# Optimization experiments

Measured on AMD Instinct MI355X. Metric: run time of the kernel, lower is better.

## Reference

```python
import jax, jax.numpy as jnp
import numpy as np

N = 100000        # nodes
E = 1600000       # directed edges
F = 602           # Reddit num_features
D = 32            # EMBEDDING_SIZE
C = 41            # Reddit num_classes
BN_EPS = 1e-5


def setup_inputs() -> dict:
    key = jax.random.key(0)
    ks = jax.random.split(key, 24)
    def w(k, shape, fan_in):
        return jax.random.normal(k, shape, dtype=jnp.float32) * (1.0 / np.sqrt(fan_in))
    inp = {
        "x": jax.random.normal(ks[0], (N, F), dtype=jnp.float32),
        "edge_index": jax.random.randint(ks[1], (2, E), 0, N, dtype=jnp.int32),
        # lin1: F -> 2*D
        "lin1_w": w(ks[2], (F, 2 * D), F), "lin1_b": jnp.zeros((2 * D,), jnp.float32),
        # conv1 MLP: 2*D -> D -> D
        "nn1_w1": w(ks[3], (2 * D, D), 2 * D), "nn1_b1": jnp.zeros((D,), jnp.float32),
        "nn1_w2": w(ks[4], (D, D), D), "nn1_b2": jnp.zeros((D,), jnp.float32),
        "bn1_g": jnp.ones((D,), jnp.float32), "bn1_b": jnp.zeros((D,), jnp.float32),
        # conv2 MLP: D -> D -> D
        "nn2_w1": w(ks[5], (D, D), D), "nn2_b1": jnp.zeros((D,), jnp.float32),
        "nn2_w2": w(ks[6], (D, D), D), "nn2_b2": jnp.zeros((D,), jnp.float32),
        "bn2_g": jnp.ones((D,), jnp.float32), "bn2_b": jnp.zeros((D,), jnp.float32),
        # heads
        "fc1_w": w(ks[7], (D, D), D), "fc1_b": jnp.zeros((D,), jnp.float32),
        "fc2_w": w(ks[8], (D, C), D), "fc2_b": jnp.zeros((C,), jnp.float32),
    }
    return inp


def _gin_conv(x, src, dst, w1, b1, w2, b2, eps=0.0):
    # sum-aggregate neighbor features (adj_t @ x) then MLP
    agg = jax.ops.segment_sum(x[src], dst, num_segments=N)  # [N, d]
    h = (1.0 + eps) * x + agg
    h = jnp.maximum(h @ w1 + b1, 0.0) @ w2 + b2
    return h


def _batch_norm(x, gamma, beta):
    # training-mode BatchNorm1d: batch statistics, biased variance
    mu = jnp.mean(x, axis=0)
    var = jnp.mean(jnp.square(x - mu), axis=0)
    return (x - mu) * jax.lax.rsqrt(var + BN_EPS) * gamma + beta


def reference(x, edge_index, lin1_w, lin1_b,
              nn1_w1, nn1_b1, nn1_w2, nn1_b2, bn1_g, bn1_b,
              nn2_w1, nn2_b1, nn2_w2, nn2_b2, bn2_g, bn2_b,
              fc1_w, fc1_b, fc2_w, fc2_b):
    src, dst = edge_index[0], edge_index[1]
    h = x @ lin1_w + lin1_b                                  # [N, 64]
    h = _batch_norm(_gin_conv(h, src, dst, nn1_w1, nn1_b1, nn1_w2, nn1_b2), bn1_g, bn1_b)
    h = _batch_norm(_gin_conv(h, src, dst, nn2_w1, nn2_b1, nn2_w2, nn2_b2), bn2_g, bn2_b)
    h = jnp.maximum(h @ fc1_w + fc1_b, 0.0)
    return h @ fc2_w + fc2_b                                 # [N, C]
```

## Files before the change

kernel.cpp:

```cpp
#include <hip/hip_runtime.h>
#include <cstdint>

#define NN 100000
#define NE 1600000
#define FI 602
#define DD 32
#define CC 41
#define BN_EPS 1e-5f
#define KSTEPS 19

#define NPB 256
#define NB 391
#define BST 4608
#define EPT 13
#define SCB 481

typedef __attribute__((ext_vector_type(8))) short bf16x8;
typedef __attribute__((ext_vector_type(4))) float f32x4;

__device__ __forceinline__ void atomAdd(float* p, float v) {
#ifdef __HIP_PLATFORM_AMD__
  unsafeAtomicAdd(p, v);
#else
  atomicAdd(p, v);
#endif
}

__device__ __forceinline__ unsigned short f2b(float f) {
  unsigned u = __float_as_uint(f);
  unsigned r = (u + 0x7fffu + ((u >> 16) & 1u)) >> 16;
  return (unsigned short)r;
}
__device__ __forceinline__ float blo(unsigned u) { return __uint_as_float(u << 16); }
__device__ __forceinline__ float bhi(unsigned u) { return __uint_as_float(u & 0xffff0000u); }

__global__ __launch_bounds__(256) void k0_prep(
    const float* __restrict__ lin1_w, const float* __restrict__ lin1_b,
    const float* __restrict__ nn1_w1,
    unsigned short* __restrict__ Bh,
    float* __restrict__ cvec,
    float* __restrict__ stats1, float* __restrict__ stats2) {
  int o = blockIdx.x * 256 + threadIdx.x;
  if (o < KSTEPS * 32 * 32) {
    int k = o >> 5, j = o & 31;
    float s = 0.f;
    if (k < FI) {
      #pragma unroll 4
      for (int c = 0; c < 2 * DD; ++c) s = fmaf(lin1_w[k * (2 * DD) + c], nn1_w1[c * DD + j], s);
    }
    int st = k >> 5, kk = k & 31, g = kk >> 3, jj = kk & 7;
    int h = j >> 4, lane = g * 16 + (j & 15);
    int idx = ((st * 2 + h) * 64 + lane) * 8 + jj;
    Bh[idx] = f2b(s);
  }
  if (blockIdx.x == 0) {
    int t = threadIdx.x;
    if (t < DD) {
      float s = 0.f;
      for (int c = 0; c < 2 * DD; ++c) s = fmaf(lin1_b[c], nn1_w1[c * DD + t], s);
      cvec[t] = s;
    }
    if (t >= 128 && t < 192) stats1[t - 128] = 0.f;
    if (t >= 192) stats2[t - 192] = 0.f;
  }
}

__global__ __launch_bounds__(256) void kb_scatter(const int* __restrict__ ei,
                                                  int* __restrict__ bcursor,
                                                  int* __restrict__ tsrc,
                                                  unsigned char* __restrict__ tdst) {
  __shared__ int cnt[NB];
  __shared__ int wbase[NB];
  const int t = threadIdx.x;
  for (int i = t; i < NB; i += 256) cnt[i] = 0;
  __syncthreads();
  const int base = blockIdx.x * (256 * EPT);
  int s[EPT], d[EPT];
  #pragma unroll
  for (int i = 0; i < EPT; ++i) {
    int e = base + i * 256 + t;
    if (e < NE) {
      s[i] = ei[e];
      d[i] = ei[NE + e];
      atomicAdd(&cnt[d[i] >> 8], 1);
    } else {
      s[i] = -1; d[i] = -1;
    }
  }
  __syncthreads();
  for (int i = t; i < NB; i += 256) wbase[i] = atomicAdd(&bcursor[i], cnt[i]);
  __syncthreads();
  #pragma unroll
  for (int i = 0; i < EPT; ++i) {
    if (d[i] >= 0) {
      int bk = d[i] >> 8;
      int p = atomicAdd(&wbase[bk], 1);
      int gp = bk * BST + p;
      tsrc[gp] = s[i];
      tdst[gp] = (unsigned char)(d[i] & (NPB - 1));
    }
  }
}

__global__ __launch_bounds__(256) void kb_fine(const int* __restrict__ bcursor,
                                               const int* __restrict__ tsrc,
                                               const unsigned char* __restrict__ tdst,
                                               int* __restrict__ rs, int* __restrict__ re,
                                               int* __restrict__ srcidx) {
  __shared__ int deg[NPB];
  __shared__ int cur[NPB];
  __shared__ int woff[4];
  const int b = blockIdx.x, t = threadIdx.x;
  const int beg = b * BST;
  const int end = beg + bcursor[b];
  deg[t] = 0;
  __syncthreads();
  for (int i = beg + t; i < end; i += 256) atomicAdd(&deg[tdst[i]], 1);
  __syncthreads();
  int v = deg[t];
  int lane = t & 63, wave = t >> 6;
  int inc = v;
  #pragma unroll
  for (int off = 1; off < 64; off <<= 1) {
    int u = __shfl_up(inc, off);
    if (lane >= off) inc += u;
  }
  if (lane == 63) woff[wave] = inc;
  __syncthreads();
  int wadd = 0;
  for (int w = 0; w < wave; ++w) wadd += woff[w];
  int excl = wadd + inc - v;
  int gnode = b * NPB + t;
  if (gnode < NN) {
    rs[gnode] = beg + excl;
    re[gnode] = beg + excl + v;
  }
  cur[t] = beg + excl;
  __syncthreads();
  for (int i = beg + t; i < end; i += 256) {
    int p = atomicAdd(&cur[tdst[i]], 1);
    srcidx[p] = tsrc[i];
  }
}

__global__ __launch_bounds__(256) void k1_mfma(
    const float* __restrict__ x,
    const unsigned short* __restrict__ Bh,
    const float* __restrict__ cvec, unsigned short* __restrict__ zb) {
  __shared__ float part[2][64][9];
  const int tid = threadIdx.x;
  const int lane = tid & 63;
  const int w = tid >> 6;
  const int rg = w & 1;
  const int kh = w >> 1;
  const int row0 = blockIdx.x * 32 + rg * 16;
  const int g = lane >> 4;
  const int r = row0 + (lane & 15);
  const float* __restrict__ xr = x + (size_t)r * FI + g * 8;
  f32x4 acc0 = {0.f, 0.f, 0.f, 0.f};
  f32x4 acc1 = {0.f, 0.f, 0.f, 0.f};

  if (kh == 0) {
    float4 a0 = *(const float4*)&xr[0];
    float4 b0 = *(const float4*)&xr[4];
    float4 a1 = *(const float4*)&xr[32];
    float4 b1 = *(const float4*)&xr[36];
    bf16x8 f0c = *(const bf16x8*)&Bh[(size_t)lane * 8];
    bf16x8 f1c = *(const bf16x8*)&Bh[(size_t)lane * 8 + 512];
    #pragma unroll
    for (int s = 0; s < 10; ++s) {
      float4 ca = a0, cb = b0;
      a0 = a1; b0 = b1;
      if (s + 2 < 10) {
        a1 = *(const float4*)&xr[(s + 2) * 32];
        b1 = *(const float4*)&xr[(s + 2) * 32 + 4];
      }
      bf16x8 f0n, f1n;
      if (s + 1 < 10) {
        const size_t fb = ((size_t)((s + 1) * 2) * 64 + lane) * 8;
        f0n = *(const bf16x8*)&Bh[fb];
        f1n = *(const bf16x8*)&Bh[fb + 512];
      }
      bf16x8 ahi, alo;
      float cv0[8] = {ca.x, ca.y, ca.z, ca.w, cb.x, cb.y, cb.z, cb.w};
      #pragma unroll
      for (int j = 0; j < 8; ++j) {
        unsigned ub = __float_as_uint(cv0[j]);
        unsigned short h = (unsigned short)(ub >> 16);
        float hv = __uint_as_float(ub & 0xffff0000u);
        float d = cv0[j] - hv;
        ahi[j] = (short)h;
        alo[j] = (short)(__float_as_uint(d) >> 16);
      }
      acc0 = __builtin_amdgcn_mfma_f32_16x16x32_bf16(ahi, f0c, acc0, 0, 0, 0);
      acc1 = __builtin_amdgcn_mfma_f32_16x16x32_bf16(ahi, f1c, acc1, 0, 0, 0);
      acc0 = __builtin_amdgcn_mfma_f32_16x16x32_bf16(alo, f0c, acc0, 0, 0, 0);
      acc1 = __builtin_amdgcn_mfma_f32_16x16x32_bf16(alo, f1c, acc1, 0, 0, 0);
      if (s + 1 < 10) { f0c = f0n; f1c = f1n; }
    }
  } else {
    float4 a0 = *(const float4*)&xr[10 * 32];
    float4 b0 = *(const float4*)&xr[10 * 32 + 4];
    float4 a1 = *(const float4*)&xr[11 * 32];
    float4 b1 = *(const float4*)&xr[11 * 32 + 4];
    bf16x8 f0c = *(const bf16x8*)&Bh[((size_t)(10 * 2) * 64 + lane) * 8];
    bf16x8 f1c = *(const bf16x8*)&Bh[((size_t)(10 * 2) * 64 + lane) * 8 + 512];
    #pragma unroll
    for (int s = 10; s < KSTEPS; ++s) {
      float4 ca = a0, cb = b0;
      a0 = a1; b0 = b1;
      if (s + 2 < KSTEPS - 1) {
        a1 = *(const float4*)&xr[(s + 2) * 32];
        b1 = *(const float4*)&xr[(s + 2) * 32 + 4];
      } else if (s + 2 == KSTEPS - 1) {
        if (g == 3) {
          float2 tt = *(const float2*)&xr[18 * 32];
          a1 = make_float4(tt.x, tt.y, 0.f, 0.f);
          b1 = make_float4(0.f, 0.f, 0.f, 0.f);
        } else {
          a1 = *(const float4*)&xr[18 * 32];
          b1 = *(const float4*)&xr[18 * 32 + 4];
        }
      }
      bf16x8 f0n, f1n;
      if (s + 1 < KSTEPS) {
        const size_t fb = ((size_t)((s + 1) * 2) * 64 + lane) * 8;
        f0n = *(const bf16x8*)&Bh[fb];
        f1n = *(const bf16x8*)&Bh[fb + 512];
      }
      bf16x8 ahi, alo;
      float cv0[8] = {ca.x, ca.y, ca.z, ca.w, cb.x, cb.y, cb.z, cb.w};
      #pragma unroll
      for (int j = 0; j < 8; ++j) {
        unsigned ub = __float_as_uint(cv0[j]);
        unsigned short h = (unsigned short)(ub >> 16);
        float hv = __uint_as_float(ub & 0xffff0000u);
        float d = cv0[j] - hv;
        ahi[j] = (short)h;
        alo[j] = (short)(__float_as_uint(d) >> 16);
      }
      acc0 = __builtin_amdgcn_mfma_f32_16x16x32_bf16(ahi, f0c, acc0, 0, 0, 0);
      acc1 = __builtin_amdgcn_mfma_f32_16x16x32_bf16(ahi, f1c, acc1, 0, 0, 0);
      acc0 = __builtin_amdgcn_mfma_f32_16x16x32_bf16(alo, f0c, acc0, 0, 0, 0);
      acc1 = __builtin_amdgcn_mfma_f32_16x16x32_bf16(alo, f1c, acc1, 0, 0, 0);
      if (s + 1 < KSTEPS) { f0c = f0n; f1c = f1n; }
    }
    #pragma unroll
    for (int j = 0; j < 4; ++j) {
      part[rg][lane][j] = acc0[j];
      part[rg][lane][4 + j] = acc1[j];
    }
  }
  __syncthreads();
  if (kh == 0) {
    const int c0 = lane & 15;
    const float cva = cvec[c0], cvb = cvec[16 + c0];
    #pragma unroll
    for (int j = 0; j < 4; ++j) {
      float v0 = acc0[j] + part[rg][lane][j] + cva;
      float v1 = acc1[j] + part[rg][lane][4 + j] + cvb;
      int rr = row0 + g * 4 + j;
      zb[(size_t)rr * DD + c0] = f2b(v0);
      zb[(size_t)rr * DD + 16 + c0] = f2b(v1);
    }
  }
}

__global__ __launch_bounds__(256) void k_gather_b(const int* __restrict__ rs,
                                                  const int* __restrict__ re,
                                                  const int* __restrict__ srcidx,
                                                  const unsigned short* __restrict__ srcb,
                                                  float* __restrict__ agg) {
  int gid = blockIdx.x * 256 + threadIdx.x;
  int n = gid >> 2, q = gid & 3;
  if (n >= NN) return;
  int beg = rs[n], end = re[n];
  float a[8] = {};
  int i = beg;
  for (; i + 8 <= end; i += 8) {
    uint4 v[8];
    #pragma unroll
    for (int j = 0; j < 8; ++j) v[j] = *(const uint4*)&srcb[(size_t)srcidx[i + j] * DD + q * 8];
    #pragma unroll
    for (int j = 0; j < 8; ++j) {
      a[0] += blo(v[j].x); a[1] += bhi(v[j].x);
      a[2] += blo(v[j].y); a[3] += bhi(v[j].y);
      a[4] += blo(v[j].z); a[5] += bhi(v[j].z);
      a[6] += blo(v[j].w); a[7] += bhi(v[j].w);
    }
  }
  for (; i + 4 <= end; i += 4) {
    uint4 v[4];
    #pragma unroll
    for (int j = 0; j < 4; ++j) v[j] = *(const uint4*)&srcb[(size_t)srcidx[i + j] * DD + q * 8];
    #pragma unroll
    for (int j = 0; j < 4; ++j) {
      a[0] += blo(v[j].x); a[1] += bhi(v[j].x);
      a[2] += blo(v[j].y); a[3] += bhi(v[j].y);
      a[4] += blo(v[j].z); a[5] += bhi(v[j].z);
      a[6] += blo(v[j].w); a[7] += bhi(v[j].w);
    }
  }
  for (; i < end; ++i) {
    uint4 v0 = *(const uint4*)&srcb[(size_t)srcidx[i] * DD + q * 8];
    a[0] += blo(v0.x); a[1] += bhi(v0.x);
    a[2] += blo(v0.y); a[3] += bhi(v0.y);
    a[4] += blo(v0.z); a[5] += bhi(v0.z);
    a[6] += blo(v0.w); a[7] += bhi(v0.w);
  }
  float* ap = &agg[(size_t)n * DD + q * 8];
  *(float4*)&ap[0] = make_float4(a[0], a[1], a[2], a[3]);
  *(float4*)&ap[4] = make_float4(a[4], a[5], a[6], a[7]);
}

__global__ __launch_bounds__(256) void k3_mlp1(
    const unsigned short* __restrict__ zb, const float* __restrict__ agg,
    const float* __restrict__ w2, const float* __restrict__ b1, const float* __restrict__ b2,
    unsigned short* __restrict__ g1b, float* __restrict__ stats) {
  __shared__ float us[256][DD + 1];
  __shared__ float w2s[DD][DD];
  __shared__ float ps[4][2 * DD];
  const int tid = threadIdx.x;
  const int n0 = blockIdx.x * 256;
  for (int i = tid; i < DD * DD; i += 256) w2s[i >> 5][i & 31] = w2[i];
  #pragma unroll
  for (int i = 0; i < 16; ++i) {
    int l = tid + i * 256;
    int r = l >> 4, c2 = l & 15;
    float lo = 0.f, hi = 0.f;
    if (n0 + r < NN) {
      size_t gi = (size_t)(n0 + r) * DD + c2 * 2;
      unsigned u = *(const unsigned*)&zb[gi];
      float2 ag = *(const float2*)&agg[gi];
      lo = blo(u) + ag.x;
      hi = bhi(u) + ag.y;
    }
    us[r][c2 * 2] = lo;
    us[r][c2 * 2 + 1] = hi;
  }
  __syncthreads();
  float t[DD];
  #pragma unroll
  for (int k = 0; k < DD; ++k) t[k] = fmaxf(us[tid][k] + b1[k], 0.f);
  float g[DD];
  #pragma unroll
  for (int j = 0; j < DD; ++j) g[j] = b2[j];
  #pragma unroll
  for (int k = 0; k < DD; ++k) {
    float tv = t[k];
    #pragma unroll
    for (int j = 0; j < DD; ++j) g[j] = fmaf(tv, w2s[k][j], g[j]);
  }
  bool valid = (n0 + tid) < NN;
  #pragma unroll
  for (int j = 0; j < DD; ++j) us[tid][j] = g[j];
  int wave = tid >> 6, lane = tid & 63;
  #pragma unroll
  for (int j = 0; j < DD; ++j) {
    float v = valid ? g[j] : 0.f;
    float qq = v * v;
    #pragma unroll
    for (int off = 1; off < 64; off <<= 1) { v += __shfl_xor(v, off); qq += __shfl_xor(qq, off); }
    if (lane == 0) { ps[wave][j] = v; ps[wave][DD + j] = qq; }
  }
  __syncthreads();
  if (tid < 2 * DD)
    atomAdd(&stats[tid], ps[0][tid] + ps[1][tid] + ps[2][tid] + ps[3][tid]);
  #pragma unroll
  for (int i = 0; i < 16; ++i) {
    int l = tid + i * 256;
    int r = l >> 4, c2 = l & 15;
    if (n0 + r < NN) {
      unsigned u = ((unsigned)f2b(us[r][c2 * 2 + 1]) << 16) | (unsigned)f2b(us[r][c2 * 2]);
      *(unsigned*)&g1b[(size_t)(n0 + r) * DD + c2 * 2] = u;
    }
  }
}

__global__ __launch_bounds__(256) void k6_mlp2(
    const unsigned short* __restrict__ g1b, const float* __restrict__ agg,
    const int* __restrict__ rsA, const int* __restrict__ reA,
    const float* __restrict__ stats1, const float* __restrict__ bn1_g, const float* __restrict__ bn1_b,
    const float* __restrict__ w1, const float* __restrict__ b1,
    const float* __restrict__ w2, const float* __restrict__ b2,
    float* __restrict__ g2, float* __restrict__ stats) {
  __shared__ float us[256][DD + 1];
  __shared__ float w1s[DD][DD];
  __shared__ float w2s[DD][DD];
  __shared__ float bns[2 * DD];
  __shared__ float ps[4][2 * DD];
  const int tid = threadIdx.x;
  const int n0 = blockIdx.x * 256;
  for (int i = tid; i < DD * DD; i += 256) { w1s[i >> 5][i & 31] = w1[i]; w2s[i >> 5][i & 31] = w2[i]; }
  if (tid < DD) {
    float mu = stats1[tid] * (1.f / NN);
    float var = stats1[DD + tid] * (1.f / NN) - mu * mu;
    float rsv = rsqrtf(var + BN_EPS) * bn1_g[tid];
    bns[tid] = rsv;
    bns[DD + tid] = bn1_b[tid] - mu * rsv;
  }
  const int n = n0 + tid;
  const bool valid = n < NN;
  float degp1 = 1.f;
  if (valid) degp1 = (float)(reA[n] - rsA[n] + 1);
  #pragma unroll
  for (int i = 0; i < 16; ++i) {
    int l = tid + i * 256;
    int r = l >> 4, c2 = l & 15;
    float lo = 0.f, hi = 0.f;
    if (n0 + r < NN) {
      size_t gi = (size_t)(n0 + r) * DD + c2 * 2;
      unsigned u = *(const unsigned*)&g1b[gi];
      float2 ag = *(const float2*)&agg[gi];
      lo = blo(u) + ag.x;
      hi = bhi(u) + ag.y;
    }
    us[r][c2 * 2] = lo;
    us[r][c2 * 2 + 1] = hi;
  }
  __syncthreads();
  float t1[DD];
  #pragma unroll
  for (int j = 0; j < DD; ++j) t1[j] = b1[j];
  #pragma unroll
  for (int k = 0; k < DD; ++k) {
    float uv = fmaf(us[tid][k], bns[k], degp1 * bns[DD + k]);
    #pragma unroll
    for (int j = 0; j < DD; ++j) t1[j] = fmaf(uv, w1s[k][j], t1[j]);
  }
  #pragma unroll
  for (int j = 0; j < DD; ++j) t1[j] = fmaxf(t1[j], 0.f);
  float g[DD];
  #pragma unroll
  for (int j = 0; j < DD; ++j) g[j] = b2[j];
  #pragma unroll
  for (int k = 0; k < DD; ++k) {
    float tv = t1[k];
    #pragma unroll
    for (int j = 0; j < DD; ++j) g[j] = fmaf(tv, w2s[k][j], g[j]);
  }
  #pragma unroll
  for (int j = 0; j < DD; ++j) us[tid][j] = g[j];
  int wave = tid >> 6, lane = tid & 63;
  #pragma unroll
  for (int j = 0; j < DD; ++j) {
    float v = valid ? g[j] : 0.f;
    float qq = v * v;
    #pragma unroll
    for (int off = 1; off < 64; off <<= 1) { v += __shfl_xor(v, off); qq += __shfl_xor(qq, off); }
    if (lane == 0) { ps[wave][j] = v; ps[wave][DD + j] = qq; }
  }
  __syncthreads();
  if (tid < 2 * DD)
    atomAdd(&stats[tid], ps[0][tid] + ps[1][tid] + ps[2][tid] + ps[3][tid]);
  #pragma unroll
  for (int i = 0; i < 32; ++i) {
    int l = tid + i * 256;
    int r = l >> 5, c = l & 31;
    if (n0 + r < NN) g2[(size_t)(n0 + r) * DD + c] = us[r][c];
  }
}

__global__ __launch_bounds__(256) void k7_head(
    const float* __restrict__ g2, const float* __restrict__ stats2,
    const float* __restrict__ bn2_g, const float* __restrict__ bn2_b,
    const float* __restrict__ fc1_w, const float* __restrict__ fc1_b,
    const float* __restrict__ fc2_w, const float* __restrict__ fc2_b,
    float* __restrict__ out) {
  __shared__ float buf[256 * 42];
  __shared__ float fc1s[DD * DD];
  __shared__ float fc2s[DD * CC];
  __shared__ float mu2[DD], rsg2[DD], bet2[DD];
  const int tid = threadIdx.x;
  const int n0 = blockIdx.x * 256;
  if (tid < DD) {
    float mu = stats2[tid] * (1.f / NN);
    float var = stats2[DD + tid] * (1.f / NN) - mu * mu;
    mu2[tid] = mu;
    rsg2[tid] = rsqrtf(var + BN_EPS) * bn2_g[tid];
    bet2[tid] = bn2_b[tid];
  }
  for (int i = tid; i < DD * DD; i += 256) fc1s[i] = fc1_w[i];
  for (int i = tid; i < DD * CC; i += 256) fc2s[i] = fc2_w[i];
  __syncthreads();
  #pragma unroll
  for (int i = 0; i < 32; ++i) {
    int l = tid + i * 256;
    int r = l >> 5, c = l & 31;
    float v = 0.f;
    if (n0 + r < NN) v = (g2[(size_t)(n0 + r) * DD + c] - mu2[c]) * rsg2[c] + bet2[c];
    buf[r * 33 + c] = v;
  }
  __syncthreads();
  float t[DD];
  #pragma unroll
  for (int j = 0; j < DD; ++j) t[j] = fc1_b[j];
  #pragma unroll
  for (int k = 0; k < DD; ++k) {
    float uv = buf[tid * 33 + k];
    #pragma unroll
    for (int j = 0; j < DD; ++j) t[j] = fmaf(uv, fc1s[k * DD + j], t[j]);
  }
  #pragma unroll
  for (int j = 0; j < DD; ++j) t[j] = fmaxf(t[j], 0.f);
  float o[CC];
  #pragma unroll
  for (int j = 0; j < CC; ++j) o[j] = fc2_b[j];
  #pragma unroll
  for (int k = 0; k < DD; ++k) {
    float tv = t[k];
    #pragma unroll
    for (int j = 0; j < CC; ++j) o[j] = fmaf(tv, fc2s[k * CC + j], o[j]);
  }
  __syncthreads();
  #pragma unroll
  for (int j = 0; j < CC; ++j) buf[tid * 42 + j] = o[j];
  __syncthreads();
  for (int i = 0; i < CC; ++i) {
    int l = tid + i * 256;
    int r = l / CC, c = l % CC;
    if (n0 + r < NN) out[(size_t)(n0 + r) * CC + c] = buf[r * 42 + c];
  }
}

extern "C" void kernel_launch(void* const* d_in, const int* in_sizes, int n_in,
                              void* d_out, int out_size, void* d_ws, size_t ws_size,
                              hipStream_t stream) {
  const float* x      = (const float*)d_in[0];
  const int*   ei     = (const int*)d_in[1];
  const float* lin1_w = (const float*)d_in[2];
  const float* lin1_b = (const float*)d_in[3];
  const float* nn1_w1 = (const float*)d_in[4];
  const float* nn1_b1 = (const float*)d_in[5];
  const float* nn1_w2 = (const float*)d_in[6];
  const float* nn1_b2 = (const float*)d_in[7];
  const float* bn1_g  = (const float*)d_in[8];
  const float* bn1_b  = (const float*)d_in[9];
  const float* nn2_w1 = (const float*)d_in[10];
  const float* nn2_b1 = (const float*)d_in[11];
  const float* nn2_w2 = (const float*)d_in[12];
  const float* nn2_b2 = (const float*)d_in[13];
  const float* bn2_g  = (const float*)d_in[14];
  const float* bn2_b  = (const float*)d_in[15];
  const float* fc1_w  = (const float*)d_in[16];
  const float* fc1_b  = (const float*)d_in[17];
  const float* fc2_w  = (const float*)d_in[18];
  const float* fc2_b  = (const float*)d_in[19];
  float* out = (float*)d_out;

  float* ws = (float*)d_ws;
  size_t nd = (size_t)NN * DD;
  float* A      = ws;
  float* B      = ws + nd;
  float* cvec   = ws + 2 * nd;
  float* stats1 = cvec + 32;
  float* stats2 = stats1 + 64;
  unsigned short* Bh = (unsigned short*)(stats2 + 64);
  int*   rsA      = (int*)(Bh + KSTEPS * 2 * 64 * 8);
  int*   reA      = rsA + NN;
  int*   srcidx   = reA + NN;
  int*   tsrc     = srcidx + (size_t)NB * BST;
  unsigned char* tdst = (unsigned char*)(tsrc + (size_t)NB * BST);
  int*   bcursor  = (int*)(tdst + (size_t)NB * BST);
  unsigned short* fb16 = (unsigned short*)tsrc;

  hipMemsetAsync(bcursor, 0, NB * sizeof(int), stream);
  kb_scatter<<<SCB, 256, 0, stream>>>(ei, bcursor, tsrc, tdst);
  kb_fine<<<NB, 256, 0, stream>>>(bcursor, tsrc, tdst, rsA, reA, srcidx);

  k0_prep<<<(KSTEPS * 32 * 32 + 255) / 256, 256, 0, stream>>>(
      lin1_w, lin1_b, nn1_w1, Bh, cvec, stats1, stats2);
  k1_mfma<<<NN / 32, 256, 0, stream>>>(x, Bh, cvec, fb16);
  k_gather_b<<<(NN * 4 + 255) / 256, 256, 0, stream>>>(rsA, reA, srcidx, fb16, B);
  k3_mlp1<<<(NN + 255) / 256, 256, 0, stream>>>(fb16, B, nn1_w2, nn1_b1, nn1_b2, fb16, stats1);
  k_gather_b<<<(NN * 4 + 255) / 256, 256, 0, stream>>>(rsA, reA, srcidx, fb16, B);
  k6_mlp2<<<(NN + 255) / 256, 256, 0, stream>>>(fb16, B, rsA, reA, stats1, bn1_g, bn1_b,
                                                nn2_w1, nn2_b1, nn2_w2, nn2_b2, A, stats2);
  k7_head<<<(NN + 255) / 256, 256, 0, stream>>>(A, stats2, bn2_g, bn2_b, fc1_w, fc1_b, fc2_w, fc2_b, out);
}
```

Baseline: 269.0 us.

## Fuse neighbor gather into GIN MLP kernels with 4-thread-per-node layout

Merges each gather kernel with its following MLP kernel, so the fp32 aggregation buffer is never written to and read back from global memory. Each node is now handled by 4 threads that each own 8 features. The matvecs exchange input values through wave shuffles instead of a per-row shared-memory tile. The first layer writes its output to a separate buffer so that in-place reads and writes do not race during the gather. In exchange, the compute stages now share occupancy with the latency-bound gather, and every k step issues a shuffle.

Result: faster. 254.4 us (-5.4%).

```diff
diff --git a/kernel.cpp b/kernel.cpp
--- a/kernel.cpp
+++ b/kernel.cpp
@@ -266,16 +266,9 @@
   }
 }
 
-__global__ __launch_bounds__(256) void k_gather_b(const int* __restrict__ rs,
-                                                  const int* __restrict__ re,
-                                                  const int* __restrict__ srcidx,
-                                                  const unsigned short* __restrict__ srcb,
-                                                  float* __restrict__ agg) {
-  int gid = blockIdx.x * 256 + threadIdx.x;
-  int n = gid >> 2, q = gid & 3;
-  if (n >= NN) return;
-  int beg = rs[n], end = re[n];
-  float a[8] = {};
+__device__ __forceinline__ void gather8(const unsigned short* __restrict__ srcb,
+                                        const int* __restrict__ srcidx,
+                                        int beg, int end, int q, float* a) {
   int i = beg;
   for (; i + 8 <= end; i += 8) {
     uint4 v[8];
@@ -308,157 +301,152 @@
     a[4] += blo(v0.z); a[5] += bhi(v0.z);
     a[6] += blo(v0.w); a[7] += bhi(v0.w);
   }
-  float* ap = &agg[(size_t)n * DD + q * 8];
-  *(float4*)&ap[0] = make_float4(a[0], a[1], a[2], a[3]);
-  *(float4*)&ap[4] = make_float4(a[4], a[5], a[6], a[7]);
-}
-
-__global__ __launch_bounds__(256) void k3_mlp1(
-    const unsigned short* __restrict__ zb, const float* __restrict__ agg,
+}
+
+__global__ __launch_bounds__(256) void k3_fused(
+    const unsigned short* __restrict__ zb,
+    const int* __restrict__ rsA, const int* __restrict__ reA,
+    const int* __restrict__ srcidx,
     const float* __restrict__ w2, const float* __restrict__ b1, const float* __restrict__ b2,
     unsigned short* __restrict__ g1b, float* __restrict__ stats) {
-  __shared__ float us[256][DD + 1];
-  __shared__ float w2s[DD][DD];
+  __shared__ float w2s[DD * DD];
+  __shared__ float b1s[DD], b2s[DD];
   __shared__ float ps[4][2 * DD];
   const int tid = threadIdx.x;
-  const int n0 = blockIdx.x * 256;
-  for (int i = tid; i < DD * DD; i += 256) w2s[i >> 5][i & 31] = w2[i];
-  #pragma unroll
-  for (int i = 0; i < 16; ++i) {
-    int l = tid + i * 256;
-    int r = l >> 4, c2 = l & 15;
-    float lo = 0.f, hi = 0.f;
-    if (n0 + r < NN) {
-      size_t gi = (size_t)(n0 + r) * DD + c2 * 2;
-      unsigned u = *(const unsigned*)&zb[gi];
-      float2 ag = *(const float2*)&agg[gi];
-      lo = blo(u) + ag.x;
-      hi = bhi(u) + ag.y;
-    }
-    us[r][c2 * 2] = lo;
-    us[r][c2 * 2 + 1] = hi;
-  }
-  __syncthreads();
-  float t[DD];
-  #pragma unroll
-  for (int k = 0; k < DD; ++k) t[k] = fmaxf(us[tid][k] + b1[k], 0.f);
-  float g[DD];
-  #pragma unroll
-  for (int j = 0; j < DD; ++j) g[j] = b2[j];
+  const int lane = tid & 63;
+  const int q = tid & 3;
+  const int n = blockIdx.x * 64 + (tid >> 2);
+  const bool valid = n < NN;
+  for (int i = tid; i < DD * DD; i += 256) w2s[i] = w2[i];
+  if (tid < DD) b1s[tid] = b1[tid];
+  else if (tid < 2 * DD) b2s[tid - DD] = b2[tid - DD];
+  __syncthreads();
+
+  float a[8] = {};
+  if (valid) {
+    uint4 v = *(const uint4*)&zb[(size_t)n * DD + q * 8];
+    a[0] = blo(v.x); a[1] = bhi(v.x); a[2] = blo(v.y); a[3] = bhi(v.y);
+    a[4] = blo(v.z); a[5] = bhi(v.z); a[6] = blo(v.w); a[7] = bhi(v.w);
+    gather8(zb, srcidx, rsA[n], reA[n], q, a);
+  }
+  float g[8];
+  #pragma unroll
+  for (int j = 0; j < 8; ++j) g[j] = b2s[q * 8 + j];
   #pragma unroll
   for (int k = 0; k < DD; ++k) {
-    float tv = t[k];
-    #pragma unroll
-    for (int j = 0; j < DD; ++j) g[j] = fmaf(tv, w2s[k][j], g[j]);
-  }
-  bool valid = (n0 + tid) < NN;
-  #pragma unroll
-  for (int j = 0; j < DD; ++j) us[tid][j] = g[j];
-  int wave = tid >> 6, lane = tid & 63;
-  #pragma unroll
-  for (int j = 0; j < DD; ++j) {
-    float v = valid ? g[j] : 0.f;
-    float qq = v * v;
-    #pragma unroll
-    for (int off = 1; off < 64; off <<= 1) { v += __shfl_xor(v, off); qq += __shfl_xor(qq, off); }
-    if (lane == 0) { ps[wave][j] = v; ps[wave][DD + j] = qq; }
+    float uv = __shfl(a[k & 7], (lane & 0x3c) | (k >> 3), 64);
+    float tv = fmaxf(uv + b1s[k], 0.f);
+    #pragma unroll
+    for (int j = 0; j < 8; ++j) g[j] = fmaf(tv, w2s[k * DD + q * 8 + j], g[j]);
+  }
+  float sv[8], sq[8];
+  #pragma unroll
+  for (int j = 0; j < 8; ++j) { sv[j] = valid ? g[j] : 0.f; sq[j] = sv[j] * sv[j]; }
+  #pragma unroll
+  for (int j = 0; j < 8; ++j) {
+    #pragma unroll
+    for (int off = 4; off < 64; off <<= 1) { sv[j] += __shfl_xor(sv[j], off); sq[j] += __shfl_xor(sq[j], off); }
+  }
+  if (lane < 4) {
+    int w = tid >> 6;
+    #pragma unroll
+    for (int j = 0; j < 8; ++j) { ps[w][q * 8 + j] = sv[j]; ps[w][DD + q * 8 + j] = sq[j]; }
+  }
+  if (valid) {
+    unsigned u0 = ((unsigned)f2b(g[1]) << 16) | f2b(g[0]);
+    unsigned u1 = ((unsigned)f2b(g[3]) << 16) | f2b(g[2]);
+    unsigned u2 = ((unsigned)f2b(g[5]) << 16) | f2b(g[4]);
+    unsigned u3 = ((unsigned)f2b(g[7]) << 16) | f2b(g[6]);
+    *(uint4*)&g1b[(size_t)n * DD + q * 8] = make_uint4(u0, u1, u2, u3);
   }
   __syncthreads();
   if (tid < 2 * DD)
     atomAdd(&stats[tid], ps[0][tid] + ps[1][tid] + ps[2][tid] + ps[3][tid]);
-  #pragma unroll
-  for (int i = 0; i < 16; ++i) {
-    int l = tid + i * 256;
-    int r = l >> 4, c2 = l & 15;
-    if (n0 + r < NN) {
-      unsigned u = ((unsigned)f2b(us[r][c2 * 2 + 1]) << 16) | (unsigned)f2b(us[r][c2 * 2]);
-      *(unsigned*)&g1b[(size_t)(n0 + r) * DD + c2 * 2] = u;
-    }
-  }
-}
-
-__global__ __launch_bounds__(256) void k6_mlp2(
-    const unsigned short* __restrict__ g1b, const float* __restrict__ agg,
+}
+
+__global__ __launch_bounds__(256) void k6_fused(
+    const unsigned short* __restrict__ g1b,
     const int* __restrict__ rsA, const int* __restrict__ reA,
+    const int* __restrict__ srcidx,
     const float* __restrict__ stats1, const float* __restrict__ bn1_g, const float* __restrict__ bn1_b,
     const float* __restrict__ w1, const float* __restrict__ b1,
     const float* __restrict__ w2, const float* __restrict__ b2,
     float* __restrict__ g2, float* __restrict__ stats) {
-  __shared__ float us[256][DD + 1];
-  __shared__ float w1s[DD][DD];
-  __shared__ float w2s[DD][DD];
+  __shared__ float w1s[DD * DD];
+  __shared__ float w2s[DD * DD];
   __shared__ float bns[2 * DD];
+  __shared__ float b1s[DD], b2s[DD];
   __shared__ float ps[4][2 * DD];
   const int tid = threadIdx.x;
-  const int n0 = blockIdx.x * 256;
-  for (int i = tid; i < DD * DD; i += 256) { w1s[i >> 5][i & 31] = w1[i]; w2s[i >> 5][i & 31] = w2[i]; }
+  const int lane = tid & 63;
+  const int q = tid & 3;
+  const int n = blockIdx.x * 64 + (tid >> 2);
+  const bool valid = n < NN;
+  for (int i = tid; i < DD * DD; i += 256) { w1s[i] = w1[i]; w2s[i] = w2[i]; }
   if (tid < DD) {
     float mu = stats1[tid] * (1.f / NN);
     float var = stats1[DD + tid] * (1.f / NN) - mu * mu;
     float rsv = rsqrtf(var + BN_EPS) * bn1_g[tid];
     bns[tid] = rsv;
     bns[DD + tid] = bn1_b[tid] - mu * rsv;
-  }
-  const int n = n0 + tid;
-  const bool valid = n < NN;
+    b1s[tid] = b1[tid];
+  } else if (tid < 2 * DD) {
+    b2s[tid - DD] = b2[tid - DD];
+  }
+  __syncthreads();
+
+  float a[8] = {};
   float degp1 = 1.f;
-  if (valid) degp1 = (float)(reA[n] - rsA[n] + 1);
-  #pragma unroll
-  for (int i = 0; i < 16; ++i) {
-    int l = tid + i * 256;
-    int r = l >> 4, c2 = l & 15;
-    float lo = 0.f, hi = 0.f;
-    if (n0 + r < NN) {
-      size_t gi = (size_t)(n0 + r) * DD + c2 * 2;
-      unsigned u = *(const unsigned*)&g1b[gi];
-      float2 ag = *(const float2*)&agg[gi];
-      lo = blo(u) + ag.x;
-      hi = bhi(u) + ag.y;
-    }
-    us[r][c2 * 2] = lo;
-    us[r][c2 * 2 + 1] = hi;
-  }
-  __syncthreads();
-  float t1[DD];
-  #pragma unroll
-  for (int j = 0; j < DD; ++j) t1[j] = b1[j];
+  if (valid) {
+    uint4 v = *(const uint4*)&g1b[(size_t)n * DD + q * 8];
+    a[0] = blo(v.x); a[1] = bhi(v.x); a[2] = blo(v.y); a[3] = bhi(v.y);
+    a[4] = blo(v.z); a[5] = bhi(v.z); a[6] = blo(v.w); a[7] = bhi(v.w);
+    int beg = rsA[n], end = reA[n];
+    degp1 = (float)(end - beg + 1);
+    gather8(g1b, srcidx, beg, end, q, a);
+  }
+  float t1[8];
+  #pragma unroll
+  for (int j = 0; j < 8; ++j) t1[j] = b1s[q * 8 + j];
   #pragma unroll
   for (int k = 0; k < DD; ++k) {
-    float uv = fmaf(us[tid][k], bns[k], degp1 * bns[DD + k]);
-    #pragma unroll
-    for (int j = 0; j < DD; ++j) t1[j] = fmaf(uv, w1s[k][j], t1[j]);
-  }
-  #pragma unroll
-  for (int j = 0; j < DD; ++j) t1[j] = fmaxf(t1[j], 0.f);
-  float g[DD];
-  #pragma unroll
-  for (int j = 0; j < DD; ++j) g[j] = b2[j];
+    float uv = __shfl(a[k & 7], (lane & 0x3c) | (k >> 3), 64);
+    float u = fmaf(uv, bns[k], degp1 * bns[DD + k]);
+    #pragma unroll
+    for (int j = 0; j < 8; ++j) t1[j] = fmaf(u, w1s[k * DD + q * 8 + j], t1[j]);
+  }
+  #pragma unroll
+  for (int j = 0; j < 8; ++j) t1[j] = fmaxf(t1[j], 0.f);
+  float g[8];
+  #pragma unroll
+  for (int j = 0; j < 8; ++j) g[j] = b2s[q * 8 + j];
   #pragma unroll
   for (int k = 0; k < DD; ++k) {
-    float tv = t1[k];
-    #pragma unroll
-    for (int j = 0; j < DD; ++j) g[j] = fmaf(tv, w2s[k][j], g[j]);
-  }
-  #pragma unroll
-  for (int j = 0; j < DD; ++j) us[tid][j] = g[j];
-  int wave = tid >> 6, lane = tid & 63;
-  #pragma unroll
-  for (int j = 0; j < DD; ++j) {
-    float v = valid ? g[j] : 0.f;
-    float qq = v * v;
-    #pragma unroll
-    for (int off = 1; off < 64; off <<= 1) { v += __shfl_xor(v, off); qq += __shfl_xor(qq, off); }
-    if (lane == 0) { ps[wave][j] = v; ps[wave][DD + j] = qq; }
+    float tv = __shfl(t1[k & 7], (lane & 0x3c) | (k >> 3), 64);
+    #pragma unroll
+    for (int j = 0; j < 8; ++j) g[j] = fmaf(tv, w2s[k * DD + q * 8 + j], g[j]);
+  }
+  float sv[8], sq[8];
+  #pragma unroll
+  for (int j = 0; j < 8; ++j) { sv[j] = valid ? g[j] : 0.f; sq[j] = sv[j] * sv[j]; }
+  #pragma unroll
+  for (int j = 0; j < 8; ++j) {
+    #pragma unroll
+    for (int off = 4; off < 64; off <<= 1) { sv[j] += __shfl_xor(sv[j], off); sq[j] += __shfl_xor(sq[j], off); }
+  }
+  if (lane < 4) {
+    int w = tid >> 6;
+    #pragma unroll
+    for (int j = 0; j < 8; ++j) { ps[w][q * 8 + j] = sv[j]; ps[w][DD + q * 8 + j] = sq[j]; }
+  }
+  if (valid) {
+    float* gp = &g2[(size_t)n * DD + q * 8];
+    *(float4*)&gp[0] = make_float4(g[0], g[1], g[2], g[3]);
+    *(float4*)&gp[4] = make_float4(g[4], g[5], g[6], g[7]);
   }
   __syncthreads();
   if (tid < 2 * DD)
     atomAdd(&stats[tid], ps[0][tid] + ps[1][tid] + ps[2][tid] + ps[3][tid]);
-  #pragma unroll
-  for (int i = 0; i < 32; ++i) {
-    int l = tid + i * 256;
-    int r = l >> 5, c = l & 31;
-    if (n0 + r < NN) g2[(size_t)(n0 + r) * DD + c] = us[r][c];
-  }
 }
 
 __global__ __launch_bounds__(256) void k7_head(
@@ -562,7 +550,8 @@
   int*   tsrc     = srcidx + (size_t)NB * BST;
   unsigned char* tdst = (unsigned char*)(tsrc + (size_t)NB * BST);
   int*   bcursor  = (int*)(tdst + (size_t)NB * BST);
-  unsigned short* fb16 = (unsigned short*)tsrc;
+  unsigned short* zb  = (unsigned short*)tsrc;
+  unsigned short* g1b = (unsigned short*)B;
 
   hipMemsetAsync(bcursor, 0, NB * sizeof(int), stream);
   kb_scatter<<<SCB, 256, 0, stream>>>(ei, bcursor, tsrc, tdst);
@@ -570,11 +559,11 @@
 
   k0_prep<<<(KSTEPS * 32 * 32 + 255) / 256, 256, 0, stream>>>(
       lin1_w, lin1_b, nn1_w1, Bh, cvec, stats1, stats2);
-  k1_mfma<<<NN / 32, 256, 0, stream>>>(x, Bh, cvec, fb16);
-  k_gather_b<<<(NN * 4 + 255) / 256, 256, 0, stream>>>(rsA, reA, srcidx, fb16, B);
-  k3_mlp1<<<(NN + 255) / 256, 256, 0, stream>>>(fb16, B, nn1_w2, nn1_b1, nn1_b2, fb16, stats1);
-  k_gather_b<<<(NN * 4 + 255) / 256, 256, 0, stream>>>(rsA, reA, srcidx, fb16, B);
-  k6_mlp2<<<(NN + 255) / 256, 256, 0, stream>>>(fb16, B, rsA, reA, stats1, bn1_g, bn1_b,
-                                                nn2_w1, nn2_b1, nn2_w2, nn2_b2, A, stats2);
+  k1_mfma<<<NN / 32, 256, 0, stream>>>(x, Bh, cvec, zb);
+  k3_fused<<<(NN + 63) / 64, 256, 0, stream>>>(zb, rsA, reA, srcidx,
+                                               nn1_w2, nn1_b1, nn1_b2, g1b, stats1);
+  k6_fused<<<(NN + 63) / 64, 256, 0, stream>>>(g1b, rsA, reA, srcidx,
+                                               stats1, bn1_g, bn1_b,
+                                               nn2_w1, nn2_b1, nn2_w2, nn2_b2, A, stats2);
   k7_head<<<(NN + 255) / 256, 256, 0, stream>>>(A, stats2, bn2_g, bn2_b, fc1_w, fc1_b, fc2_w, fc2_b, out);
 }
```
